# Kernel optimization log

Measured on AMD Instinct MI355X. Metric: run time of the kernel, lower is better.

Reference implementation:

```python
import jax, jax.numpy as jnp
import numpy as np

B, S, IN, H, D, M, OUT, TOPK = 4, 256, 256, 512, 128, 100000, 256, 3
EPS = 1e-12  # F.normalize eps


def _l2norm(x):
    n = jnp.sqrt(jnp.sum(x * x, axis=-1, keepdims=True))
    return x / jnp.maximum(n, EPS)


def setup_inputs() -> dict:
    key = jax.random.key(0)
    ks = jax.random.split(key, 16)
    s = 0.02
    return {
        "x": jax.random.normal(ks[0], (B, S, IN), jnp.float32),
        # LSTM params (torch gate order i,f,g,o)
        "W_ih": jax.random.normal(ks[1], (4 * H, IN), jnp.float32) * s,
        "W_hh": jax.random.normal(ks[2], (4 * H, H), jnp.float32) * s,
        "b_ih": jax.random.normal(ks[3], (4 * H,), jnp.float32) * s,
        "b_hh": jax.random.normal(ks[4], (4 * H,), jnp.float32) * s,
        # memory interface
        "Wq": jax.random.normal(ks[5], (D, H), jnp.float32) * s,
        "bq": jax.random.normal(ks[6], (D,), jnp.float32) * s,
        "Wa": jax.random.normal(ks[7], (1, D), jnp.float32) * s,
        "ba": jax.random.normal(ks[8], (1,), jnp.float32) * s,
        "Wc": jax.random.normal(ks[9], (D, D), jnp.float32) * s,
        "bc": jax.random.normal(ks[10], (D,), jnp.float32) * s,
        # output layer
        "Wo": jax.random.normal(ks[11], (OUT, H + D), jnp.float32) * s,
        "bo": jax.random.normal(ks[12], (OUT,), jnp.float32) * s,
        # memory bank (importance_weight == 1.0 for all fresh entries)
        "mem_keys": jax.random.normal(ks[13], (M, D), jnp.float32),
        "mem_values": jax.random.normal(ks[14], (M, D), jnp.float32),
    }


def _lstm(x, W_ih, W_hh, b_ih, b_hh):
    b = b_ih + b_hh
    xg = jnp.einsum('bsi,gi->bsg', x, W_ih) + b  # (B,S,4H)

    def step(carry, xg_t):
        h, c = carry
        g = xg_t + h @ W_hh.T
        i, f, gg, o = jnp.split(g, 4, axis=-1)
        c = jax.nn.sigmoid(f) * c + jax.nn.sigmoid(i) * jnp.tanh(gg)
        h = jax.nn.sigmoid(o) * jnp.tanh(c)
        return (h, c), h

    h0 = jnp.zeros((x.shape[0], W_hh.shape[1]), x.dtype)
    (_, _), hs = jax.lax.scan(step, (h0, h0), jnp.swapaxes(xg, 0, 1))
    return jnp.swapaxes(hs, 0, 1)  # (B,S,H)


def reference(x, W_ih, W_hh, b_ih, b_hh, Wq, bq, Wa, ba, Wc, bc, Wo, bo, mem_keys, mem_values):
    h = _lstm(x, W_ih, W_hh, b_ih, b_hh)               # (B,S,H)
    q = _l2norm(h @ Wq.T + bq)                          # (B,S,D) normalized query
    kn = _l2norm(mem_keys)                              # (M,D)
    sims = jnp.einsum('bsd,md->bsm', q, kn)             # cosine sims (x1.0 importance)
    _, idx = jax.lax.top_k(sims, TOPK)                  # (B,S,K)
    retrieved = mem_values[idx]                         # (B,S,K,D) gather
    att = jax.nn.softmax(jnp.squeeze(retrieved @ Wa.T + ba, -1), axis=-1)  # (B,S,K)
    mem = jnp.einsum('bsk,bskd->bsd', att, retrieved)
    mem = mem @ Wc.T + bc                               # combine_layer
    out = jnp.concatenate([h, mem], axis=-1) @ Wo.T + bo  # (B,S,OUT)
    return out
```

## Files before the change

kernel.cpp:

```cpp
#include <hip/hip_runtime.h>
#include <math.h>

#define INF __builtin_inff()
#define SENT 0x7FA00000u
#define IMAX 0x7fffffff

typedef __attribute__((ext_vector_type(8))) short bhalf8;
typedef __attribute__((ext_vector_type(4))) float f32x4;


__device__ __forceinline__ void ins3b(float& v0, int& i0, float& v1, int& i1,
                                      float& v2, int& i2, float nv, int ni) {
  bool b0 = (nv > v0) || (nv == v0 && ni < i0);
  bool b1 = (nv > v1) || (nv == v1 && ni < i1);
  bool b2 = (nv > v2) || (nv == v2 && ni < i2);
  v2 = b1 ? v1 : (b2 ? nv : v2);
  i2 = b1 ? i1 : (b2 ? ni : i2);
  v1 = b0 ? v0 : (b1 ? nv : v1);
  i1 = b0 ? i0 : (b1 ? ni : i1);
  v0 = b0 ? nv : v0;
  i0 = b0 ? ni : i0;
}

__device__ __forceinline__ unsigned short f2bf(float x) {
  unsigned u = __float_as_uint(x);
  return (unsigned short)((u + 0x7FFFu + ((u >> 16) & 1u)) >> 16);
}

__global__ void init_k(float* __restrict__ h_seq, unsigned* __restrict__ flags) {
  int t = blockIdx.x * 256 + threadIdx.x;
  if (t < 526336) h_seq[t] = (t < 2048) ? 0.f : __uint_as_float(SENT);
  if (t < 16) flags[t] = 0u;
}

template<int AMODE>
__global__ __launch_bounds__(256) void gemm_k(
    const float* __restrict__ A, const float* __restrict__ A2,
    const float* __restrict__ Bw, const float* __restrict__ b1,
    const float* __restrict__ b2, float* __restrict__ C,
    int M, int N, int K) {
  __shared__ float4 As4[64][16];
  __shared__ float4 Bs4[64][16];
  const int t = threadIdx.x;
  const int tx = t & 15, ty = t >> 4;
  const int brow = blockIdx.x * 64, bcol = blockIdx.y * 64;
  const int srow = t >> 2, scb = t & 3;
  float acc[4][4] = {};
  for (int kt = 0; kt < K; kt += 64) {
#pragma unroll
    for (int u = 0; u < 4; ++u) {
      int c = scb + 4 * u;
      int gk = kt + c * 4;
      int gr = brow + srow;
      const float* ap;
      if (AMODE == 0) {
        ap = A + (size_t)gr * K + gk;
      } else {
        int b = gr >> 8, s = gr & 255;
        const float* hrow = A + ((size_t)(s + 1) * 4 + b) * 512;
        if (AMODE == 1) ap = hrow + gk;
        else ap = (gk < 512) ? (hrow + gk) : (A2 + (size_t)gr * 128 + (gk - 512));
      }
      As4[srow][c ^ (srow & 15)] = *(const float4*)ap;
      Bs4[srow][c ^ (srow & 15)] = *(const float4*)(Bw + (size_t)(bcol + srow) * K + gk);
    }
    __syncthreads();
#pragma unroll
    for (int d4 = 0; d4 < 16; ++d4) {
      float4 av[4], bv[4];
#pragma unroll
      for (int i = 0; i < 4; ++i) av[i] = As4[ty * 4 + i][d4 ^ ((ty * 4 + i) & 15)];
#pragma unroll
      for (int j = 0; j < 4; ++j) bv[j] = Bs4[tx * 4 + j][d4 ^ ((tx * 4 + j) & 15)];
#pragma unroll
      for (int i = 0; i < 4; ++i)
#pragma unroll
        for (int j = 0; j < 4; ++j)
          acc[i][j] += av[i].x * bv[j].x + av[i].y * bv[j].y +
                       av[i].z * bv[j].z + av[i].w * bv[j].w;
    }
    __syncthreads();
  }
#pragma unroll
  for (int i = 0; i < 4; ++i) {
    int r = brow + ty * 4 + i;
#pragma unroll
    for (int j = 0; j < 4; ++j) {
      int n = bcol + tx * 4 + j;
      float bias = b1[n];
      if (b2) bias += b2[n];
      C[(size_t)r * N + n] = acc[i][j] + bias;
    }
  }
}

__global__ __launch_bounds__(512, 2) void fused_front(
    const float* __restrict__ x, const float* __restrict__ W_ih,
    const float* __restrict__ b_ih, const float* __restrict__ b_hh,
    const float* __restrict__ W_hh, const float* __restrict__ keys,
    float* __restrict__ xg, float* __restrict__ h_seq,
    float* __restrict__ invn, unsigned* __restrict__ kbf,
    unsigned* __restrict__ xgflag) {
  __shared__ alignas(16) unsigned char smem[32768];
  const int bid = blockIdx.x;
  const int t = threadIdx.x;

  if (bid < 64) {
    const int batch = bid >> 4;
    const int ub = bid & 15;
    const int uu = t >> 4;
    const int li = t & 15;
    const int unit = ub * 32 + uu;
    float* h_lds = (float*)smem;

    float w[4][32];
#pragma unroll
    for (int g = 0; g < 4; ++g) {
      const float* wr = W_hh + (size_t)(g * 512 + unit) * 512 + li * 32;
#pragma unroll
      for (int j = 0; j < 32; j += 4) {
        float4 v = *(const float4*)(wr + j);
        w[g][j] = v.x; w[g][j + 1] = v.y; w[g][j + 2] = v.z; w[g][j + 3] = v.w;
      }
    }
    float c = 0.f;
    {
      const unsigned* f0 = xgflag + batch * 4;
      while (__hip_atomic_load(f0, __ATOMIC_RELAXED, __HIP_MEMORY_SCOPE_AGENT) < 32u) {}
      (void)__hip_atomic_load(f0, __ATOMIC_ACQUIRE, __HIP_MEMORY_SCOPE_AGENT);
    }
    float xcur[4], xnxt[4];
    {
      const float* xq = xg + (size_t)(batch * 256) * 2048 + unit;
#pragma unroll
      for (int g = 0; g < 4; ++g) xcur[g] = xq[g * 512];
#pragma unroll
      for (int g = 0; g < 4; ++g) xnxt[g] = xq[2048 + g * 512];
    }

    for (int step = 0; step < 256; ++step) {
      {
        float* hp = h_seq + ((size_t)step * 4 + batch) * 512 + t;
        float hv;
        do {
          hv = __hip_atomic_load(hp, __ATOMIC_RELAXED, __HIP_MEMORY_SCOPE_AGENT);
        } while (__float_as_uint(hv) == SENT);
        h_lds[(step & 1) * 576 + (t >> 5) * 36 + (t & 31)] = hv;
      }
      __syncthreads();
      const float* hb = h_lds + (step & 1) * 576 + li * 36;
      float a0 = 0.f, a1 = 0.f, a2 = 0.f, a3 = 0.f;
#pragma unroll
      for (int j = 0; j < 32; j += 4) {
        float4 hv = *(const float4*)(hb + j);
        a0 += w[0][j] * hv.x + w[0][j + 1] * hv.y + w[0][j + 2] * hv.z + w[0][j + 3] * hv.w;
        a1 += w[1][j] * hv.x + w[1][j + 1] * hv.y + w[1][j + 2] * hv.z + w[1][j + 3] * hv.w;
        a2 += w[2][j] * hv.x + w[2][j + 1] * hv.y + w[2][j + 2] * hv.z + w[2][j + 3] * hv.w;
        a3 += w[3][j] * hv.x + w[3][j + 1] * hv.y + w[3][j + 2] * hv.z + w[3][j + 3] * hv.w;
      }
#pragma unroll
      for (int m = 1; m < 16; m <<= 1) {
        a0 += __shfl_xor(a0, m, 64); a1 += __shfl_xor(a1, m, 64);
        a2 += __shfl_xor(a2, m, 64); a3 += __shfl_xor(a3, m, 64);
      }
      a0 += xcur[0]; a1 += xcur[1]; a2 += xcur[2]; a3 += xcur[3];
      float i_ = 1.f / (1.f + expf(-a0));
      float f_ = 1.f / (1.f + expf(-a1));
      float g_ = tanhf(a2);
      float o_ = 1.f / (1.f + expf(-a3));
      c = f_ * c + i_ * g_;
      float h = o_ * tanhf(c);
      if (li == 0)
        __hip_atomic_store(h_seq + ((size_t)(step + 1) * 4 + batch) * 512 + unit,
                           h, __ATOMIC_RELAXED, __HIP_MEMORY_SCOPE_AGENT);
#pragma unroll
      for (int g = 0; g < 4; ++g) xcur[g] = xnxt[g];
      if (step + 2 < 256) {
        if (((step + 2) & 63) == 0) {
          const unsigned* fq = xgflag + batch * 4 + ((step + 2) >> 6);
          while (__hip_atomic_load(fq, __ATOMIC_RELAXED, __HIP_MEMORY_SCOPE_AGENT) < 32u) {}
          (void)__hip_atomic_load(fq, __ATOMIC_ACQUIRE, __HIP_MEMORY_SCOPE_AGENT);
        }
        const float* xq = xg + (size_t)(batch * 256 + step + 2) * 2048 + unit;
#pragma unroll
        for (int g = 0; g < 4; ++g) xnxt[g] = xq[g * 512];
      }
    }
  } else if (bid < 576) {
    const int g = bid - 64;
    const int q = g >> 7;
    const int b = (g >> 5) & 3;
    const int col = g & 31;
    const int brow = (b * 4 + q) * 64, bcol = col * 64;
    float4* As4 = (float4*)smem;
    float4* Bs4 = (float4*)(smem + 16384);
    const int tx = t & 15, ty = (t >> 4) & 15;
    const int srow = (t & 255) >> 2, scb = t & 3;
    float acc[4][4] = {};
    for (int kt = 0; kt < 256; kt += 64) {
      if (t < 256) {
#pragma unroll
        for (int u = 0; u < 4; ++u) {
          int cc = scb + 4 * u;
          int gk = kt + cc * 4;
          As4[srow * 16 + (cc ^ (srow & 15))] =
              *(const float4*)(x + (size_t)(brow + srow) * 256 + gk);
          Bs4[srow * 16 + (cc ^ (srow & 15))] =
              *(const float4*)(W_ih + (size_t)(bcol + srow) * 256 + gk);
        }
      }
      __syncthreads();
      if (t < 256) {
#pragma unroll
        for (int d4 = 0; d4 < 16; ++d4) {
          float4 av[4], bv[4];
#pragma unroll
          for (int i = 0; i < 4; ++i)
            av[i] = As4[(ty * 4 + i) * 16 + (d4 ^ ((ty * 4 + i) & 15))];
#pragma unroll
          for (int j = 0; j < 4; ++j)
            bv[j] = Bs4[(tx * 4 + j) * 16 + (d4 ^ ((tx * 4 + j) & 15))];
#pragma unroll
          for (int i = 0; i < 4; ++i)
#pragma unroll
            for (int j = 0; j < 4; ++j)
              acc[i][j] += av[i].x * bv[j].x + av[i].y * bv[j].y +
                           av[i].z * bv[j].z + av[i].w * bv[j].w;
        }
      }
      __syncthreads();
    }
    if (t < 256) {
#pragma unroll
      for (int i = 0; i < 4; ++i) {
        int r = brow + ty * 4 + i;
#pragma unroll
        for (int j = 0; j < 4; ++j) {
          int n = bcol + tx * 4 + j;
          xg[(size_t)r * 2048 + n] = acc[i][j] + b_ih[n] + b_hh[n];
        }
      }
    }
    __syncthreads();
    if (t == 0)
      __hip_atomic_fetch_add(xgflag + b * 4 + q, 1u, __ATOMIC_RELEASE,
                             __HIP_MEMORY_SCOPE_AGENT);
  } else {
    const int rb = (bid - 576) * 256;
    const int wv = t >> 6, lane = t & 63;
    for (int p = 0; p < 32; ++p) {
      int r = rb + p * 8 + wv;
      if (r < 100000) {
        float2 v = *(const float2*)(keys + (size_t)r * 128 + lane * 2);
        float ss = v.x * v.x + v.y * v.y;
#pragma unroll
        for (int m = 1; m < 64; m <<= 1) ss += __shfl_xor(ss, m, 64);
        float inv = 1.f / fmaxf(sqrtf(ss), 1e-12f);
        if (lane == 0) invn[r] = inv;
        kbf[(size_t)r * 64 + lane] =
            (unsigned)f2bf(v.x * inv) | ((unsigned)f2bf(v.y * inv) << 16);
      }
    }
  }
}

__global__ __launch_bounds__(256) void qnorm_k(float* __restrict__ q,
                                               unsigned* __restrict__ qbf) {
  int wv = threadIdx.x >> 6, lane = threadIdx.x & 63;
  int r = blockIdx.x * 4 + wv;
  float2 v = *(float2*)(q + (size_t)r * 128 + lane * 2);
  float ss = v.x * v.x + v.y * v.y;
#pragma unroll
  for (int m = 1; m < 64; m <<= 1) ss += __shfl_xor(ss, m, 64);
  float inv = 1.f / fmaxf(sqrtf(ss), 1e-12f);
  v.x *= inv; v.y *= inv;
  *(float2*)(q + (size_t)r * 128 + lane * 2) = v;
  qbf[(size_t)r * 64 + lane] = (unsigned)f2bf(v.x) | ((unsigned)f2bf(v.y) << 16);
}

__device__ __forceinline__ void stage_tile(unsigned short* dst,
                                           const unsigned* src,
                                           int baserow, int maxrow,
                                           int w, int l) {
#pragma unroll
  for (int u = 0; u < 4; ++u) {
    int s = u * 256 + w * 64 + l;
    int row = s >> 4, cc = s & 15;
    int gr = baserow + row; gr = gr > maxrow ? maxrow : gr;
    const unsigned* sp = src + (size_t)gr * 64 + ((cc ^ (row & 7)) << 2);
    __builtin_amdgcn_global_load_lds(
        (const __attribute__((address_space(1))) unsigned*)sp,
        (__attribute__((address_space(3))) unsigned*)(dst + (size_t)(u * 256 + w * 64) * 8),
        16, 0, 0);
  }
}

__global__ __launch_bounds__(256, 2) void simsmfma_k(
    const unsigned* __restrict__ qbf, const unsigned* __restrict__ kbf,
    float* __restrict__ pvals, int* __restrict__ pidx) {
  const int qt = blockIdx.x, ch = blockIdx.y;
  const int kbeg = ch * 3125, klim = kbeg + 3125;
  const int t = threadIdx.x, l = t & 63, w = t >> 6;
  __shared__ alignas(16) unsigned short ks0[8192];
  __shared__ alignas(16) unsigned short ks1[8192];

  stage_tile(ks1, qbf, qt * 64, 1023, w, l);
  __syncthreads();
  bhalf8 afrag[4];
  {
    int row = w * 16 + (l & 15);
#pragma unroll
    for (int db = 0; db < 4; ++db) {
      int cslot = db * 4 + (l >> 4);
      afrag[db] = *(const bhalf8*)&ks1[(size_t)(row * 16 + (cslot ^ (row & 7))) * 8];
    }
  }
  stage_tile(ks0, kbf, kbeg, klim - 1, w, l);
  __syncthreads();

  float tv0[4], tv1[4], tv2[4]; int ti0[4], ti1[4], ti2[4];
#pragma unroll
  for (int r = 0; r < 4; ++r) {
    tv0[r] = tv1[r] = tv2[r] = -INF;
    ti0[r] = ti1[r] = ti2[r] = IMAX;
  }

  for (int s = 0; s < 49; ++s) {
    unsigned short* cur = (s & 1) ? ks1 : ks0;
    unsigned short* nxt = (s & 1) ? ks0 : ks1;
    if (s < 48) stage_tile(nxt, kbf, kbeg + (s + 1) * 64, klim - 1, w, l);
    int k0 = kbeg + s * 64;

    f32x4 ac0 = {0,0,0,0}, ac1 = {0,0,0,0}, ac2 = {0,0,0,0}, ac3 = {0,0,0,0};
    const int r0 = l & 15;
#pragma unroll
    for (int db = 0; db < 4; ++db) {
      int swz = (db * 4 + (l >> 4)) ^ (r0 & 7);
      bhalf8 b0 = *(const bhalf8*)&cur[(size_t)((r0     ) * 16 + swz) * 8];
      bhalf8 b1 = *(const bhalf8*)&cur[(size_t)((r0 + 16) * 16 + swz) * 8];
      bhalf8 b2 = *(const bhalf8*)&cur[(size_t)((r0 + 32) * 16 + swz) * 8];
      bhalf8 b3 = *(const bhalf8*)&cur[(size_t)((r0 + 48) * 16 + swz) * 8];
      ac0 = __builtin_amdgcn_mfma_f32_16x16x32_bf16(afrag[db], b0, ac0, 0, 0, 0);
      ac1 = __builtin_amdgcn_mfma_f32_16x16x32_bf16(afrag[db], b1, ac1, 0, 0, 0);
      ac2 = __builtin_amdgcn_mfma_f32_16x16x32_bf16(afrag[db], b2, ac2, 0, 0, 0);
      ac3 = __builtin_amdgcn_mfma_f32_16x16x32_bf16(afrag[db], b3, ac3, 0, 0, 0);
    }
#pragma unroll
    for (int nt = 0; nt < 4; ++nt) {
      f32x4 a = (nt == 0) ? ac0 : (nt == 1) ? ac1 : (nt == 2) ? ac2 : ac3;
      int gk = k0 + nt * 16 + (l & 15);
      bool ok = gk < klim;
#pragma unroll
      for (int r = 0; r < 4; ++r) {
        float v = ok ? a[r] : -INF;
        ins3b(tv0[r], ti0[r], tv1[r], ti1[r], tv2[r], ti2[r], v, gk);
      }
    }
    __syncthreads();
  }

#pragma unroll
  for (int r = 0; r < 4; ++r) {
    float c0 = tv0[r], c1 = tv1[r], c2 = tv2[r];
    int j0 = ti0[r], j1 = ti1[r], j2 = ti2[r];
    int qrow = qt * 64 + w * 16 + (l >> 4) * 4 + r;
    size_t ob = ((size_t)ch * 1024 + qrow) * 6;
#pragma unroll
    for (int e = 0; e < 6; ++e) {
      float mv = c0; int mi = j0;
#pragma unroll
      for (int m = 1; m < 16; m <<= 1) {
        float o = __shfl_xor(mv, m, 64); int oi = __shfl_xor(mi, m, 64);
        bool tk = (o > mv) || (o == mv && oi < mi);
        mv = tk ? o : mv; mi = tk ? oi : mi;
      }
      if (mi == j0) { c0 = c1; j0 = j1; c1 = c2; j1 = j2; c2 = -INF; j2 = IMAX; }
      if ((l & 15) == 0) { pvals[ob + e] = mv; pidx[ob + e] = mi; }
    }
  }
}

__global__ __launch_bounds__(256) void merge_rescore_k(
    const float* __restrict__ pvals, const int* __restrict__ pidx,
    const float* __restrict__ qf, const float* __restrict__ keys,
    const float* __restrict__ invn, const float* __restrict__ mvals,
    const float* __restrict__ Wa, const float* __restrict__ ba,
    float* __restrict__ mem_pre) {
  int wv = threadIdx.x >> 6, l = threadIdx.x & 63;
  int qr = blockIdx.x * 4 + wv;
  float h0 = -INF, h1 = -INF, h2 = -INF;
  int g0 = IMAX, g1 = IMAX, g2 = IMAX;
#pragma unroll
  for (int e = 0; e < 3; ++e) {
    int c = l * 3 + e;
    size_t base = ((size_t)(c / 6) * 1024 + qr) * 6 + (c % 6);
    ins3b(h0, g0, h1, g1, h2, g2, pvals[base], pidx[base]);
  }
  float sc[8]; int si[8];
#pragma unroll
  for (int e = 0; e < 8; ++e) {
    float mv = h0; int mi = g0;
#pragma unroll
    for (int m = 1; m < 64; m <<= 1) {
      float o = __shfl_xor(mv, m, 64); int oi = __shfl_xor(mi, m, 64);
      bool tk = (o > mv) || (o == mv && oi < mi);
      mv = tk ? o : mv; mi = tk ? oi : mi;
    }
    sc[e] = mv; si[e] = mi;
    if (mi == g0) { h0 = h1; g0 = g1; h1 = h2; g1 = g2; h2 = -INF; g2 = IMAX; }
  }
  int d = l * 2;
  float q0 = qf[(size_t)qr * 128 + d], q1 = qf[(size_t)qr * 128 + d + 1];
  float ex[8];
#pragma unroll
  for (int e = 0; e < 8; ++e) {
    int k = si[e];
    float p = q0 * keys[(size_t)k * 128 + d] + q1 * keys[(size_t)k * 128 + d + 1];
#pragma unroll
    for (int m = 1; m < 64; m <<= 1) p += __shfl_xor(p, m, 64);
    ex[e] = p * invn[k];
  }
  float v0 = -INF, v1 = -INF, v2 = -INF;
  int i0 = IMAX, i1 = IMAX, i2 = IMAX;
#pragma unroll
  for (int e = 0; e < 8; ++e) ins3b(v0, i0, v1, i1, v2, i2, ex[e], si[e]);
  float r00 = mvals[(size_t)i0 * 128 + d], r01 = mvals[(size_t)i0 * 128 + d + 1];
  float r10 = mvals[(size_t)i1 * 128 + d], r11 = mvals[(size_t)i1 * 128 + d + 1];
  float r20 = mvals[(size_t)i2 * 128 + d], r21 = mvals[(size_t)i2 * 128 + d + 1];
  float wa0 = Wa[d], wa1 = Wa[d + 1];
  float p0 = wa0 * r00 + wa1 * r01;
  float p1 = wa0 * r10 + wa1 * r11;
  float p2 = wa0 * r20 + wa1 * r21;
#pragma unroll
  for (int m = 1; m < 64; m <<= 1) {
    p0 += __shfl_xor(p0, m, 64);
    p1 += __shfl_xor(p1, m, 64);
    p2 += __shfl_xor(p2, m, 64);
  }
  float bav = ba[0];
  float l0 = p0 + bav, l1 = p1 + bav, l2 = p2 + bav;
  float mx = fmaxf(l0, fmaxf(l1, l2));
  float e0 = expf(l0 - mx), e1 = expf(l1 - mx), e2 = expf(l2 - mx);
  float s = e0 + e1 + e2;
  float a0 = e0 / s, a1 = e1 / s, a2 = e2 / s;
  mem_pre[(size_t)qr * 128 + d]     = a0 * r00 + a1 * r10 + a2 * r20;
  mem_pre[(size_t)qr * 128 + d + 1] = a0 * r01 + a1 * r11 + a2 * r21;
}

extern "C" void kernel_launch(void* const* d_in, const int* in_sizes, int n_in,
                              void* d_out, int out_size, void* d_ws, size_t ws_size,
                              hipStream_t stream) {
  (void)in_sizes; (void)n_in; (void)out_size; (void)ws_size;
  const float* x    = (const float*)d_in[0];
  const float* W_ih = (const float*)d_in[1];
  const float* W_hh = (const float*)d_in[2];
  const float* b_ih = (const float*)d_in[3];
  const float* b_hh = (const float*)d_in[4];
  const float* Wq   = (const float*)d_in[5];
  const float* bq   = (const float*)d_in[6];
  const float* Wa   = (const float*)d_in[7];
  const float* ba   = (const float*)d_in[8];
  const float* Wc   = (const float*)d_in[9];
  const float* bc   = (const float*)d_in[10];
  const float* Wo   = (const float*)d_in[11];
  const float* bo   = (const float*)d_in[12];
  const float* keys = (const float*)d_in[13];
  const float* vals = (const float*)d_in[14];

  float* ws      = (float*)d_ws;
  float* xg      = ws + 0;
  float* h_seq   = ws + 2097152;
  float* qbuf    = ws + 2623488;
  float* invn    = ws + 2754560;
  float* mem_pre = ws + 2854560;
  float* mem_cmb = ws + 2985632;
  float* pvals   = ws + 3116704;
  int*   pidx    = (int*)(ws + 3313312);
  unsigned* qbf  = (unsigned*)(ws + 3509920);
  unsigned* kbf  = (unsigned*)(ws + 3575456);
  unsigned* xgflag = (unsigned*)pvals;

  init_k<<<2056, 256, 0, stream>>>(h_seq, xgflag);
  fused_front<<<967, 512, 0, stream>>>(x, W_ih, b_ih, b_hh, W_hh, keys,
                                       xg, h_seq, invn, kbf, xgflag);
  gemm_k<1><<<dim3(16, 2), 256, 0, stream>>>(h_seq, nullptr, Wq, bq, nullptr,
                                             qbuf, 1024, 128, 512);
  qnorm_k<<<256, 256, 0, stream>>>(qbuf, qbf);
  simsmfma_k<<<dim3(16, 32), 256, 0, stream>>>(qbf, kbf, pvals, pidx);
  merge_rescore_k<<<256, 256, 0, stream>>>(pvals, pidx, qbuf, keys, invn, vals,
                                           Wa, ba, mem_pre);
  gemm_k<0><<<dim3(16, 2), 256, 0, stream>>>(mem_pre, nullptr, Wc, bc, nullptr,
                                             mem_cmb, 1024, 128, 128);
  gemm_k<2><<<dim3(16, 4), 256, 0, stream>>>(h_seq, mem_cmb, Wo, bo, nullptr,
                                             (float*)d_out, 1024, 256, 640);
}
```

Before: 1.133 ms.

## Fuse query projection, normalization and similarity top-k into the persistent LSTM kernel

Adds 16 query-projection blocks and 512 similarity/top-k blocks to the fused front kernel. The projection blocks poll h_seq sentinels so each 64-row query tile is projected and L2-normalized as soon as its timesteps are produced. The similarity blocks wait on per-tile and key-normalization flags, which lets top-k work overlap the serial LSTM recurrence and removes three kernel launches. The costs are more shared memory per block and idle upper waves in the sim blocks. Spinning blocks that hold CU slots could also starve or slow the recurrence blocks.

```diff
diff --git a/kernel.cpp b/kernel.cpp
--- a/kernel.cpp
+++ b/kernel.cpp
@@ -27,10 +27,17 @@
   return (unsigned short)((u + 0x7FFFu + ((u >> 16) & 1u)) >> 16);
 }
 
+__device__ __forceinline__ float pollf(const float* p) {
+  float v;
+  do { v = __hip_atomic_load(p, __ATOMIC_RELAXED, __HIP_MEMORY_SCOPE_AGENT); }
+  while (__float_as_uint(v) == SENT);
+  return v;
+}
+
 __global__ void init_k(float* __restrict__ h_seq, unsigned* __restrict__ flags) {
   int t = blockIdx.x * 256 + threadIdx.x;
   if (t < 526336) h_seq[t] = (t < 2048) ? 0.f : __uint_as_float(SENT);
-  if (t < 16) flags[t] = 0u;
+  if (t < 33) flags[t] = 0u;
 }
 
 template<int AMODE>
@@ -58,8 +65,7 @@
       } else {
         int b = gr >> 8, s = gr & 255;
         const float* hrow = A + ((size_t)(s + 1) * 4 + b) * 512;
-        if (AMODE == 1) ap = hrow + gk;
-        else ap = (gk < 512) ? (hrow + gk) : (A2 + (size_t)gr * 128 + (gk - 512));
+        ap = (gk < 512) ? (hrow + gk) : (A2 + (size_t)gr * 128 + (gk - 512));
       }
       As4[srow][c ^ (srow & 15)] = *(const float4*)ap;
       Bs4[srow][c ^ (srow & 15)] = *(const float4*)(Bw + (size_t)(bcol + srow) * K + gk);
@@ -94,16 +100,39 @@
   }
 }
 
+__device__ __forceinline__ void stage_tile(unsigned short* dst,
+                                           const unsigned* src,
+                                           int baserow, int maxrow,
+                                           int w, int l) {
+#pragma unroll
+  for (int u = 0; u < 4; ++u) {
+    int s = u * 256 + w * 64 + l;
+    int row = s >> 4, cc = s & 15;
+    int gr = baserow + row; gr = gr > maxrow ? maxrow : gr;
+    const unsigned* sp = src + (size_t)gr * 64 + ((cc ^ (row & 7)) << 2);
+    __builtin_amdgcn_global_load_lds(
+        (const __attribute__((address_space(1))) unsigned*)sp,
+        (__attribute__((address_space(3))) unsigned*)(dst + (size_t)(u * 256 + w * 64) * 8),
+        16, 0, 0);
+  }
+}
+
 __global__ __launch_bounds__(512, 2) void fused_front(
     const float* __restrict__ x, const float* __restrict__ W_ih,
     const float* __restrict__ b_ih, const float* __restrict__ b_hh,
     const float* __restrict__ W_hh, const float* __restrict__ keys,
+    const float* __restrict__ Wq, const float* __restrict__ bq,
     float* __restrict__ xg, float* __restrict__ h_seq,
     float* __restrict__ invn, unsigned* __restrict__ kbf,
-    unsigned* __restrict__ xgflag) {
-  __shared__ alignas(16) unsigned char smem[32768];
+    float* __restrict__ qbuf, unsigned* __restrict__ qbf,
+    float* __restrict__ pvals, int* __restrict__ pidx,
+    unsigned* __restrict__ flags) {
+  __shared__ alignas(16) unsigned char smem[49152];
   const int bid = blockIdx.x;
   const int t = threadIdx.x;
+  unsigned* xgflag = flags;
+  unsigned* qflag  = flags + 16;
+  unsigned* kcflag = flags + 32;
 
   if (bid < 64) {
     const int batch = bid >> 4;
@@ -140,11 +169,7 @@
 
     for (int step = 0; step < 256; ++step) {
       {
-        float* hp = h_seq + ((size_t)step * 4 + batch) * 512 + t;
-        float hv;
-        do {
-          hv = __hip_atomic_load(hp, __ATOMIC_RELAXED, __HIP_MEMORY_SCOPE_AGENT);
-        } while (__float_as_uint(hv) == SENT);
+        float hv = pollf(h_seq + ((size_t)step * 4 + batch) * 512 + t);
         h_lds[(step & 1) * 576 + (t >> 5) * 36 + (t & 31)] = hv;
       }
       __syncthreads();
@@ -245,7 +270,7 @@
     if (t == 0)
       __hip_atomic_fetch_add(xgflag + b * 4 + q, 1u, __ATOMIC_RELEASE,
                              __HIP_MEMORY_SCOPE_AGENT);
-  } else {
+  } else if (bid < 967) {
     const int rb = (bid - 576) * 256;
     const int wv = t >> 6, lane = t & 63;
     for (int p = 0; p < 32; ++p) {
@@ -261,121 +286,196 @@
             (unsigned)f2bf(v.x * inv) | ((unsigned)f2bf(v.y * inv) << 16);
       }
     }
-  }
-}
-
-__global__ __launch_bounds__(256) void qnorm_k(float* __restrict__ q,
-                                               unsigned* __restrict__ qbf) {
-  int wv = threadIdx.x >> 6, lane = threadIdx.x & 63;
-  int r = blockIdx.x * 4 + wv;
-  float2 v = *(float2*)(q + (size_t)r * 128 + lane * 2);
-  float ss = v.x * v.x + v.y * v.y;
-#pragma unroll
-  for (int m = 1; m < 64; m <<= 1) ss += __shfl_xor(ss, m, 64);
-  float inv = 1.f / fmaxf(sqrtf(ss), 1e-12f);
-  v.x *= inv; v.y *= inv;
-  *(float2*)(q + (size_t)r * 128 + lane * 2) = v;
-  qbf[(size_t)r * 64 + lane] = (unsigned)f2bf(v.x) | ((unsigned)f2bf(v.y) << 16);
-}
-
-__device__ __forceinline__ void stage_tile(unsigned short* dst,
-                                           const unsigned* src,
-                                           int baserow, int maxrow,
-                                           int w, int l) {
-#pragma unroll
-  for (int u = 0; u < 4; ++u) {
-    int s = u * 256 + w * 64 + l;
-    int row = s >> 4, cc = s & 15;
-    int gr = baserow + row; gr = gr > maxrow ? maxrow : gr;
-    const unsigned* sp = src + (size_t)gr * 64 + ((cc ^ (row & 7)) << 2);
-    __builtin_amdgcn_global_load_lds(
-        (const __attribute__((address_space(1))) unsigned*)sp,
-        (__attribute__((address_space(3))) unsigned*)(dst + (size_t)(u * 256 + w * 64) * 8),
-        16, 0, 0);
-  }
-}
-
-__global__ __launch_bounds__(256, 2) void simsmfma_k(
-    const unsigned* __restrict__ qbf, const unsigned* __restrict__ kbf,
-    float* __restrict__ pvals, int* __restrict__ pidx) {
-  const int qt = blockIdx.x, ch = blockIdx.y;
-  const int kbeg = ch * 3125, klim = kbeg + 3125;
-  const int t = threadIdx.x, l = t & 63, w = t >> 6;
-  __shared__ alignas(16) unsigned short ks0[8192];
-  __shared__ alignas(16) unsigned short ks1[8192];
-
-  stage_tile(ks1, qbf, qt * 64, 1023, w, l);
-  __syncthreads();
-  bhalf8 afrag[4];
-  {
-    int row = w * 16 + (l & 15);
-#pragma unroll
-    for (int db = 0; db < 4; ++db) {
-      int cslot = db * 4 + (l >> 4);
-      afrag[db] = *(const bhalf8*)&ks1[(size_t)(row * 16 + (cslot ^ (row & 7))) * 8];
-    }
-  }
-  stage_tile(ks0, kbf, kbeg, klim - 1, w, l);
-  __syncthreads();
-
-  float tv0[4], tv1[4], tv2[4]; int ti0[4], ti1[4], ti2[4];
-#pragma unroll
-  for (int r = 0; r < 4; ++r) {
-    tv0[r] = tv1[r] = tv2[r] = -INF;
-    ti0[r] = ti1[r] = ti2[r] = IMAX;
-  }
-
-  for (int s = 0; s < 49; ++s) {
-    unsigned short* cur = (s & 1) ? ks1 : ks0;
-    unsigned short* nxt = (s & 1) ? ks0 : ks1;
-    if (s < 48) stage_tile(nxt, kbf, kbeg + (s + 1) * 64, klim - 1, w, l);
-    int k0 = kbeg + s * 64;
-
-    f32x4 ac0 = {0,0,0,0}, ac1 = {0,0,0,0}, ac2 = {0,0,0,0}, ac3 = {0,0,0,0};
-    const int r0 = l & 15;
-#pragma unroll
-    for (int db = 0; db < 4; ++db) {
-      int swz = (db * 4 + (l >> 4)) ^ (r0 & 7);
-      bhalf8 b0 = *(const bhalf8*)&cur[(size_t)((r0     ) * 16 + swz) * 8];
-      bhalf8 b1 = *(const bhalf8*)&cur[(size_t)((r0 + 16) * 16 + swz) * 8];
-      bhalf8 b2 = *(const bhalf8*)&cur[(size_t)((r0 + 32) * 16 + swz) * 8];
-      bhalf8 b3 = *(const bhalf8*)&cur[(size_t)((r0 + 48) * 16 + swz) * 8];
-      ac0 = __builtin_amdgcn_mfma_f32_16x16x32_bf16(afrag[db], b0, ac0, 0, 0, 0);
-      ac1 = __builtin_amdgcn_mfma_f32_16x16x32_bf16(afrag[db], b1, ac1, 0, 0, 0);
-      ac2 = __builtin_amdgcn_mfma_f32_16x16x32_bf16(afrag[db], b2, ac2, 0, 0, 0);
-      ac3 = __builtin_amdgcn_mfma_f32_16x16x32_bf16(afrag[db], b3, ac3, 0, 0, 0);
-    }
-#pragma unroll
-    for (int nt = 0; nt < 4; ++nt) {
-      f32x4 a = (nt == 0) ? ac0 : (nt == 1) ? ac1 : (nt == 2) ? ac2 : ac3;
-      int gk = k0 + nt * 16 + (l & 15);
-      bool ok = gk < klim;
+    __syncthreads();
+    if (t == 0)
+      __hip_atomic_fetch_add(kcflag, 1u, __ATOMIC_RELEASE,
+                             __HIP_MEMORY_SCOPE_AGENT);
+  } else if (bid < 983) {
+    const int qt = bid - 967;
+    const int b = qt >> 2;
+    const int s0 = (qt & 3) * 64;
+    float4* A4 = (float4*)smem;
+    float4* B4 = (float4*)(smem + 16384);
+    const int tx = t & 15, ty = (t >> 4) & 15;
+    float acc[4][8] = {};
+    for (int kt = 0; kt < 512; kt += 64) {
+      if (t < 256) {
+#pragma unroll
+        for (int u = 0; u < 4; ++u) {
+          int p = t + 256 * u;
+          int row = p >> 4, c4 = p & 15;
+          const float* hp = h_seq + ((size_t)(s0 + row + 1) * 4 + b) * 512 + kt + c4 * 4;
+          float4 v;
+          v.x = pollf(hp + 0); v.y = pollf(hp + 1);
+          v.z = pollf(hp + 2); v.w = pollf(hp + 3);
+          A4[row * 16 + (c4 ^ (row & 15))] = v;
+        }
+#pragma unroll
+        for (int u = 0; u < 8; ++u) {
+          int p = t + 256 * u;
+          int row = p >> 4, c4 = p & 15;
+          B4[row * 16 + (c4 ^ (row & 15))] =
+              *(const float4*)(Wq + (size_t)row * 512 + kt + c4 * 4);
+        }
+      }
+      __syncthreads();
+      if (t < 256) {
+#pragma unroll
+        for (int d4 = 0; d4 < 16; ++d4) {
+          float4 av[4], bv[8];
+#pragma unroll
+          for (int i = 0; i < 4; ++i)
+            av[i] = A4[(ty * 4 + i) * 16 + (d4 ^ ((ty * 4 + i) & 15))];
+#pragma unroll
+          for (int j = 0; j < 8; ++j)
+            bv[j] = B4[(tx * 8 + j) * 16 + (d4 ^ ((tx * 8 + j) & 15))];
+#pragma unroll
+          for (int i = 0; i < 4; ++i)
+#pragma unroll
+            for (int j = 0; j < 8; ++j)
+              acc[i][j] += av[i].x * bv[j].x + av[i].y * bv[j].y +
+                           av[i].z * bv[j].z + av[i].w * bv[j].w;
+        }
+      }
+      __syncthreads();
+    }
+    float* part = (float*)smem;
+    float* invq = (float*)(smem + 4096);
+    if (t < 256) {
+#pragma unroll
+      for (int i = 0; i < 4; ++i) {
+        float ss = 0.f;
+#pragma unroll
+        for (int j = 0; j < 8; ++j) {
+          acc[i][j] += bq[tx * 8 + j];
+          ss += acc[i][j] * acc[i][j];
+        }
+        part[(ty * 4 + i) * 16 + tx] = ss;
+      }
+    }
+    __syncthreads();
+    if (t < 64) {
+      float ss = 0.f;
+#pragma unroll
+      for (int x2 = 0; x2 < 16; ++x2) ss += part[t * 16 + x2];
+      invq[t] = 1.f / fmaxf(sqrtf(ss), 1e-12f);
+    }
+    __syncthreads();
+    if (t < 256) {
+#pragma unroll
+      for (int i = 0; i < 4; ++i) {
+        int r = qt * 64 + ty * 4 + i;
+        float inv = invq[ty * 4 + i];
+        float o[8];
+#pragma unroll
+        for (int j = 0; j < 8; ++j) o[j] = acc[i][j] * inv;
+        *(float4*)(qbuf + (size_t)r * 128 + tx * 8) =
+            make_float4(o[0], o[1], o[2], o[3]);
+        *(float4*)(qbuf + (size_t)r * 128 + tx * 8 + 4) =
+            make_float4(o[4], o[5], o[6], o[7]);
+#pragma unroll
+        for (int j2 = 0; j2 < 4; ++j2)
+          qbf[(size_t)r * 64 + tx * 4 + j2] =
+              (unsigned)f2bf(o[j2 * 2]) | ((unsigned)f2bf(o[j2 * 2 + 1]) << 16);
+      }
+    }
+    __syncthreads();
+    if (t == 0)
+      __hip_atomic_fetch_add(qflag + qt, 1u, __ATOMIC_RELEASE,
+                             __HIP_MEMORY_SCOPE_AGENT);
+  } else {
+    const int sidx = bid - 983;
+    const int qt = sidx >> 5, ch = sidx & 31;
+    const int kbeg = ch * 3125, klim = kbeg + 3125;
+    const int l = t & 63, w4 = t >> 6;
+    unsigned short* ks0 = (unsigned short*)smem;
+    unsigned short* ks1 = (unsigned short*)(smem + 16384);
+
+    if (t == 0) {
+      while (__hip_atomic_load(kcflag, __ATOMIC_RELAXED, __HIP_MEMORY_SCOPE_AGENT) < 391u)
+        __builtin_amdgcn_s_sleep(8);
+      while (__hip_atomic_load(qflag + qt, __ATOMIC_RELAXED, __HIP_MEMORY_SCOPE_AGENT) < 1u)
+        __builtin_amdgcn_s_sleep(8);
+      (void)__hip_atomic_load(qflag + qt, __ATOMIC_ACQUIRE, __HIP_MEMORY_SCOPE_AGENT);
+    }
+    __syncthreads();
+
+    if (w4 < 4) stage_tile(ks1, qbf, qt * 64, 1023, w4, l);
+    __syncthreads();
+    bhalf8 afrag[4];
+    if (w4 < 4) {
+      int row = w4 * 16 + (l & 15);
+#pragma unroll
+      for (int db = 0; db < 4; ++db) {
+        int cslot = db * 4 + (l >> 4);
+        afrag[db] = *(const bhalf8*)&ks1[(size_t)(row * 16 + (cslot ^ (row & 7))) * 8];
+      }
+      stage_tile(ks0, kbf, kbeg, klim - 1, w4, l);
+    }
+    __syncthreads();
+
+    float tv0[4], tv1[4], tv2[4]; int ti0[4], ti1[4], ti2[4];
+#pragma unroll
+    for (int r = 0; r < 4; ++r) {
+      tv0[r] = tv1[r] = tv2[r] = -INF;
+      ti0[r] = ti1[r] = ti2[r] = IMAX;
+    }
+
+    for (int s = 0; s < 49; ++s) {
+      if (w4 < 4) {
+        unsigned short* cur = (s & 1) ? ks1 : ks0;
+        unsigned short* nxt = (s & 1) ? ks0 : ks1;
+        if (s < 48) stage_tile(nxt, kbf, kbeg + (s + 1) * 64, klim - 1, w4, l);
+        int k0 = kbeg + s * 64;
+        f32x4 ac0 = {0,0,0,0}, ac1 = {0,0,0,0}, ac2 = {0,0,0,0}, ac3 = {0,0,0,0};
+        const int r0 = l & 15;
+#pragma unroll
+        for (int db = 0; db < 4; ++db) {
+          int swz = (db * 4 + (l >> 4)) ^ (r0 & 7);
+          bhalf8 b0 = *(const bhalf8*)&cur[(size_t)((r0     ) * 16 + swz) * 8];
+          bhalf8 b1 = *(const bhalf8*)&cur[(size_t)((r0 + 16) * 16 + swz) * 8];
+          bhalf8 b2 = *(const bhalf8*)&cur[(size_t)((r0 + 32) * 16 + swz) * 8];
+          bhalf8 b3 = *(const bhalf8*)&cur[(size_t)((r0 + 48) * 16 + swz) * 8];
+          ac0 = __builtin_amdgcn_mfma_f32_16x16x32_bf16(afrag[db], b0, ac0, 0, 0, 0);
+          ac1 = __builtin_amdgcn_mfma_f32_16x16x32_bf16(afrag[db], b1, ac1, 0, 0, 0);
+          ac2 = __builtin_amdgcn_mfma_f32_16x16x32_bf16(afrag[db], b2, ac2, 0, 0, 0);
+          ac3 = __builtin_amdgcn_mfma_f32_16x16x32_bf16(afrag[db], b3, ac3, 0, 0, 0);
+        }
+#pragma unroll
+        for (int nt = 0; nt < 4; ++nt) {
+          f32x4 a = (nt == 0) ? ac0 : (nt == 1) ? ac1 : (nt == 2) ? ac2 : ac3;
+          int gk = k0 + nt * 16 + (l & 15);
+          bool ok = gk < klim;
+#pragma unroll
+          for (int r = 0; r < 4; ++r) {
+            float v = ok ? a[r] : -INF;
+            ins3b(tv0[r], ti0[r], tv1[r], ti1[r], tv2[r], ti2[r], v, gk);
+          }
+        }
+      }
+      __syncthreads();
+    }
+
+    if (w4 < 4) {
 #pragma unroll
       for (int r = 0; r < 4; ++r) {
-        float v = ok ? a[r] : -INF;
-        ins3b(tv0[r], ti0[r], tv1[r], ti1[r], tv2[r], ti2[r], v, gk);
-      }
-    }
-    __syncthreads();
-  }
-
-#pragma unroll
-  for (int r = 0; r < 4; ++r) {
-    float c0 = tv0[r], c1 = tv1[r], c2 = tv2[r];
-    int j0 = ti0[r], j1 = ti1[r], j2 = ti2[r];
-    int qrow = qt * 64 + w * 16 + (l >> 4) * 4 + r;
-    size_t ob = ((size_t)ch * 1024 + qrow) * 6;
-#pragma unroll
-    for (int e = 0; e < 6; ++e) {
-      float mv = c0; int mi = j0;
-#pragma unroll
-      for (int m = 1; m < 16; m <<= 1) {
-        float o = __shfl_xor(mv, m, 64); int oi = __shfl_xor(mi, m, 64);
-        bool tk = (o > mv) || (o == mv && oi < mi);
-        mv = tk ? o : mv; mi = tk ? oi : mi;
-      }
-      if (mi == j0) { c0 = c1; j0 = j1; c1 = c2; j1 = j2; c2 = -INF; j2 = IMAX; }
-      if ((l & 15) == 0) { pvals[ob + e] = mv; pidx[ob + e] = mi; }
+        float c0 = tv0[r], c1 = tv1[r], c2 = tv2[r];
+        int j0 = ti0[r], j1 = ti1[r], j2 = ti2[r];
+        int qrow = qt * 64 + w4 * 16 + (l >> 4) * 4 + r;
+        size_t ob = ((size_t)ch * 1024 + qrow) * 6;
+#pragma unroll
+        for (int e = 0; e < 6; ++e) {
+          float mv = c0; int mi = j0;
+#pragma unroll
+          for (int m = 1; m < 16; m <<= 1) {
+            float o = __shfl_xor(mv, m, 64); int oi = __shfl_xor(mi, m, 64);
+            bool tk = (o > mv) || (o == mv && oi < mi);
+            mv = tk ? o : mv; mi = tk ? oi : mi;
+          }
+          if (mi == j0) { c0 = c1; j0 = j1; c1 = c2; j1 = j2; c2 = -INF; j2 = IMAX; }
+          if ((l & 15) == 0) { pvals[ob + e] = mv; pidx[ob + e] = mi; }
+        }
+      }
     }
   }
 }
@@ -478,15 +578,12 @@
   int*   pidx    = (int*)(ws + 3313312);
   unsigned* qbf  = (unsigned*)(ws + 3509920);
   unsigned* kbf  = (unsigned*)(ws + 3575456);
-  unsigned* xgflag = (unsigned*)pvals;
-
-  init_k<<<2056, 256, 0, stream>>>(h_seq, xgflag);
-  fused_front<<<967, 512, 0, stream>>>(x, W_ih, b_ih, b_hh, W_hh, keys,
-                                       xg, h_seq, invn, kbf, xgflag);
-  gemm_k<1><<<dim3(16, 2), 256, 0, stream>>>(h_seq, nullptr, Wq, bq, nullptr,
-                                             qbuf, 1024, 128, 512);
-  qnorm_k<<<256, 256, 0, stream>>>(qbuf, qbf);
-  simsmfma_k<<<dim3(16, 32), 256, 0, stream>>>(qbf, kbf, pvals, pidx);
+  unsigned* flags = (unsigned*)mem_cmb;
+
+  init_k<<<2056, 256, 0, stream>>>(h_seq, flags);
+  fused_front<<<1495, 512, 0, stream>>>(x, W_ih, b_ih, b_hh, W_hh, keys, Wq, bq,
+                                        xg, h_seq, invn, kbf, qbuf, qbf,
+                                        pvals, pidx, flags);
   merge_rescore_k<<<256, 256, 0, stream>>>(pvals, pidx, qbuf, keys, invn, vals,
                                            Wa, ba, mem_pre);
   gemm_k<0><<<dim3(16, 2), 256, 0, stream>>>(mem_pre, nullptr, Wc, bc, nullptr,
```

Measured after the change: 1.514 ms. 1.34x slower.
